# Optimization experiments

Measured on AMD Instinct MI355X. Metric: run time of the kernel, lower is better.

Reference implementation:

```python
import jax, jax.numpy as jnp
import numpy as np

B, N, M, D = 32, 500, 500, 256
SQRT_D = 16.0
LOGIT_CLIP = 10.0


def setup_inputs() -> dict:
    key = jax.random.key(0)
    ks = jax.random.split(key, 12)
    s = 1.0 / np.sqrt(D)
    return {
        "encoded_q0": jax.random.normal(ks[0], (B, N, D), jnp.float32),
        "encoded_jobs": jax.random.normal(ks[1], (B, M, D), jnp.float32),
        "encoded_q1": jax.random.normal(ks[2], (B, N, D), jnp.float32),
        "cur_cost_mat": jax.random.uniform(ks[3], (B, N, M), jnp.float32),
        "log_scale": jnp.ones((1,), jnp.float32),
        "ninf_mask": jnp.zeros((B, N, M), jnp.float32),
        "Wq0": jax.random.normal(ks[4], (D, D), jnp.float32) * s,
        "Wq1": jax.random.normal(ks[5], (D, D), jnp.float32) * s,
        "Wk": jax.random.normal(ks[6], (D, D), jnp.float32) * s,
        "Wv": jax.random.normal(ks[7], (D, D), jnp.float32) * s,
        "alpha1": jnp.ones((1,), jnp.float32),
        "alpha2": jnp.ones((1,), jnp.float32),
    }


def reference(encoded_q0, encoded_jobs, encoded_q1, cur_cost_mat, log_scale,
              ninf_mask, Wq0, Wq1, Wk, Wv, alpha1, alpha2):
    # precomputed state (set_kv / set_q1): Linear without bias -> x @ W.T
    k = jnp.einsum('bmd,ed->bme', encoded_jobs, Wk)
    v = jnp.einsum('bmd,ed->bme', encoded_jobs, Wv)
    q1 = jnp.einsum('bnd,ed->bne', encoded_q1, Wq1)
    q0 = jnp.einsum('bnd,ed->bne', encoded_q0, Wq0)
    q = q1 + q0

    # AAFM: adaptation bias = -alpha1 * log_scale * cost (+ ninf_mask)
    exp_bias = jnp.exp(-alpha1 * log_scale * cur_cost_mat + ninf_mask)  # (B,N,M)
    exp_k = jnp.exp(k)                                                   # (B,M,D)
    num = jnp.einsum('bnm,bmd->bnd', exp_bias, exp_k * v)
    den = jnp.einsum('bnm,bmd->bnd', exp_bias, exp_k)
    weighted = jnp.nan_to_num(num / den)
    aafm_out = jax.nn.sigmoid(q) * weighted                              # (B,N,D)

    # single-head scoring against raw encoded_jobs
    score = jnp.einsum('bnd,bmd->bnm', aafm_out, encoded_jobs)
    score = score / SQRT_D - alpha2 * log_scale * cur_cost_mat
    score = LOGIT_CLIP * jnp.tanh(score) + ninf_mask
    return jax.nn.softmax(score, axis=-1)
```

## Files before the change

### kernel.cpp

```cpp
#include <hip/hip_runtime.h>
#include <math.h>

using u16 = unsigned short;
typedef __attribute__((ext_vector_type(8))) short short8;
typedef __attribute__((ext_vector_type(16))) float floatx16;

constexpr int Bc = 32, Nn = 500, Mm = 500, Dd = 256;
constexpr float LOGIT_CLIP = 10.0f;
constexpr float INV_SQRT_D = 1.0f / 16.0f;

__device__ __forceinline__ floatx16 mfma32(short8 a, short8 b, floatx16 c) {
    return __builtin_amdgcn_mfma_f32_32x32x16_bf16(a, b, c, 0, 0, 0);
}

__device__ __forceinline__ floatx16 zero16() {
    floatx16 v = {0.f,0.f,0.f,0.f,0.f,0.f,0.f,0.f,0.f,0.f,0.f,0.f,0.f,0.f,0.f,0.f};
    return v;
}

__device__ __forceinline__ void gl_lds16(const u16* g, u16* l) {
    __builtin_amdgcn_global_load_lds(
        (const __attribute__((address_space(1))) unsigned int*)g,
        (__attribute__((address_space(3))) unsigned int*)l, 16, 0, 0);
}

__device__ __forceinline__ void split1(float x, u16& h, u16& l) {
    unsigned u = __float_as_uint(x);
    unsigned rh = (u + 0x7FFFu + ((u >> 16) & 1u)) & 0xFFFF0000u;
    float fh = __uint_as_float(rh);
    float fl = x - fh;
    unsigned ul = __float_as_uint(fl);
    unsigned rl = ul + 0x7FFFu + ((ul >> 16) & 1u);
    h = (u16)(rh >> 16);
    l = (u16)(rl >> 16);
}

__device__ __forceinline__ u16 bf16rtn(float x) {
    unsigned u = __float_as_uint(x);
    return (u16)((u + 0x7FFFu + ((u >> 16) & 1u)) >> 16);
}

__device__ __forceinline__ float fast_tanh(float x) {
    return 1.0f - 2.0f / (__expf(2.0f * x) + 1.0f);
}

__device__ __forceinline__ void split8(const float4& a, const float4& c,
                                       short8& hv, short8& lv) {
    u16 hh, ll;
    split1(a.x, hh, ll); hv[0] = (short)hh; lv[0] = (short)ll;
    split1(a.y, hh, ll); hv[1] = (short)hh; lv[1] = (short)ll;
    split1(a.z, hh, ll); hv[2] = (short)hh; lv[2] = (short)ll;
    split1(a.w, hh, ll); hv[3] = (short)hh; lv[3] = (short)ll;
    split1(c.x, hh, ll); hv[4] = (short)hh; lv[4] = (short)ll;
    split1(c.y, hh, ll); hv[5] = (short)hh; lv[5] = (short)ll;
    split1(c.z, hh, ll); hv[6] = (short)hh; lv[6] = (short)ll;
    split1(c.w, hh, ll); hv[7] = (short)hh; lv[7] = (short)ll;
}


__global__ __launch_bounds__(256) void k0w_pk(const float* __restrict__ s0,
                                              const float* __restrict__ s1,
                                              const float* __restrict__ s2,
                                              const float* __restrict__ s3,
                                              u16* __restrict__ pkw) {
    const float* s = blockIdx.y == 0 ? s0 : blockIdx.y == 1 ? s1 :
                     blockIdx.y == 2 ? s2 : s3;
    const int w = blockIdx.y;
    const int flat = (blockIdx.x * 256 + threadIdx.x) * 8;
    const int i = flat >> 8, j0 = flat & 255;
    float4 a = *(const float4*)&s[flat];
    float4 c = *(const float4*)&s[flat + 4];
    short8 hv, lv;
    split8(a, c, hv, lv);
    const int dt = i >> 5, i31 = i & 31, dc = j0 >> 4, hp = (j0 >> 3) & 1;
    const size_t off = (size_t)(w * 8 + dt) * 16384 + (size_t)dc * 1024
                     + (size_t)((hp << 5) | i31) * 8;
    *(short8*)&pkw[off] = hv;
    *(short8*)&pkw[off + 512] = lv;
}

__global__ __launch_bounds__(256) void k0pkj(const float* __restrict__ s,
                                             u16* __restrict__ d) {
    const int bx = blockIdx.x;
    const int b = bx >> 6;
    const int chunk = bx & 63;
    const int flat = threadIdx.x * 8;
    const int lr = flat >> 8;
    const int j0 = flat & 255;
    const int pr = chunk * 8 + lr;
    short8 hv = {0,0,0,0,0,0,0,0}, lv = {0,0,0,0,0,0,0,0};
    if (pr < Nn) {
        const size_t o = ((size_t)b * Nn + pr) * Dd + j0;
        float4 a = *(const float4*)&s[o];
        float4 c = *(const float4*)&s[o + 4];
        split8(a, c, hv, lv);
    }
    const int mt = pr >> 5, r31 = pr & 31;
    const int dc = j0 >> 4, hp = (j0 >> 3) & 1;
    const size_t off = (size_t)(b * 16 + mt) * 16384 + (size_t)dc * 1024
                     + (size_t)((hp << 5) | r31) * 8;
    *(short8*)&d[off] = hv;
    *(short8*)&d[off + 512] = lv;
}

__global__ __launch_bounds__(256) void k1_kv(const u16* __restrict__ pkj,
                                             const u16* __restrict__ pkw,
                                             u16* __restrict__ pkb) {
    const int lane = threadIdx.x & 63, wv = threadIdx.x >> 6;
    const int l31 = lane & 31, h = lane >> 5;
    const int b = blockIdx.z;
    const int dt = blockIdx.y * 4 + wv;
    const int mt = blockIdx.x;
    const int M0 = mt * 32;

    const size_t wk  = (size_t)dt * 16384 + (size_t)lane * 8;
    const size_t wvb = (size_t)(8 + dt) * 16384 + (size_t)lane * 8;
    const size_t jb  = (size_t)(b * 16 + mt) * 16384 + (size_t)lane * 8;

    floatx16 ak = zero16(), av = zero16();

    short8 buf[3][6];
#define K1L(S, DC) { \
    buf[S][0] = *(const short8*)(pkw + wk  + (size_t)(DC) * 1024); \
    buf[S][1] = *(const short8*)(pkw + wk  + (size_t)(DC) * 1024 + 512); \
    buf[S][2] = *(const short8*)(pkw + wvb + (size_t)(DC) * 1024); \
    buf[S][3] = *(const short8*)(pkw + wvb + (size_t)(DC) * 1024 + 512); \
    buf[S][4] = *(const short8*)(pkj + jb  + (size_t)(DC) * 1024); \
    buf[S][5] = *(const short8*)(pkj + jb  + (size_t)(DC) * 1024 + 512); }

    K1L(0, 0)
    K1L(1, 1)
#pragma unroll
    for (int it = 0; it < 16; ++it) {
        if (it + 2 < 16) { K1L((it + 2) % 3, it + 2) }
        const int c = it % 3;
        ak = mfma32(buf[c][0], buf[c][4], ak);
        ak = mfma32(buf[c][0], buf[c][5], ak);
        ak = mfma32(buf[c][1], buf[c][4], ak);
        av = mfma32(buf[c][2], buf[c][4], av);
        av = mfma32(buf[c][2], buf[c][5], av);
        av = mfma32(buf[c][3], buf[c][4], av);
    }
#undef K1L

    const int hp = (l31 >> 3) & 1, ee = l31 & 7, mcl = l31 >> 4;
    const size_t sb0 = ((size_t)b * 8 + dt) * 65536
                     + (size_t)(mt * 2 + mcl) * 2048 + (size_t)hp * 256 + ee;
    const bool v0 = (M0 + l31) < Mm;
#pragma unroll
    for (int r = 0; r < 16; ++r) {
        const int d31 = (r & 3) + ((r >> 2) << 3) + (h << 2);
        const size_t o = sb0 + (size_t)d31 * 8;
        u16 hh, ll;
        const float ek = v0 ? __expf(ak[r]) : 0.f;
        const float ev = v0 ? ek * av[r] : 0.f;
        split1(ek, hh, ll); pkb[o] = hh; pkb[o + 512] = ll;
        split1(ev, hh, ll); pkb[o + 1024] = hh; pkb[o + 1536] = ll;
    }
}

__global__ __launch_bounds__(256) void k2_q(const float* __restrict__ q0,
                                            const float* __restrict__ q1,
                                            const u16* __restrict__ pkw,
                                            float* __restrict__ sq) {
    __shared__ u16 tq[4][32][264];
    const int t = threadIdx.x;
    const int lane = t & 63, wv = t >> 6;
    const int l31 = lane & 31, h = lane >> 5;
    const int b = blockIdx.y;
    const int nt = blockIdx.x;

#pragma unroll
    for (int s = 0; s < 2; ++s) {
        const float* src = s ? q1 : q0;
#pragma unroll
        for (int it = 0; it < 4; ++it) {
            const int flat = (it * 256 + t) * 8;
            const int nl = flat >> 8, j0 = flat & 255;
            const int n = min(nt * 32 + nl, Nn - 1);
            const size_t o = ((size_t)b * Nn + n) * Dd + j0;
            float4 a = *(const float4*)&src[o];
            float4 c = *(const float4*)&src[o + 4];
            short8 hv, lv;
            split8(a, c, hv, lv);
            *(short8*)&tq[s * 2][nl][j0] = hv;
            *(short8*)&tq[s * 2 + 1][nl][j0] = lv;
        }
    }
    __syncthreads();

    const int dt0 = wv;
    const int dt1 = wv + 4;
    const size_t w00 = (size_t)(16 + dt0) * 16384 + (size_t)lane * 8;
    const size_t w10 = (size_t)(24 + dt0) * 16384 + (size_t)lane * 8;
    const size_t w01 = (size_t)(16 + dt1) * 16384 + (size_t)lane * 8;
    const size_t w11 = (size_t)(24 + dt1) * 16384 + (size_t)lane * 8;

    floatx16 acc0 = zero16(), acc1 = zero16();

    short8 buf[3][8];
#define K2L(S, DC) { \
    buf[S][0] = *(const short8*)(pkw + w00 + (size_t)(DC) * 1024); \
    buf[S][1] = *(const short8*)(pkw + w00 + (size_t)(DC) * 1024 + 512); \
    buf[S][2] = *(const short8*)(pkw + w10 + (size_t)(DC) * 1024); \
    buf[S][3] = *(const short8*)(pkw + w10 + (size_t)(DC) * 1024 + 512); \
    buf[S][4] = *(const short8*)(pkw + w01 + (size_t)(DC) * 1024); \
    buf[S][5] = *(const short8*)(pkw + w01 + (size_t)(DC) * 1024 + 512); \
    buf[S][6] = *(const short8*)(pkw + w11 + (size_t)(DC) * 1024); \
    buf[S][7] = *(const short8*)(pkw + w11 + (size_t)(DC) * 1024 + 512); }

    K2L(0, 0)
    K2L(1, 1)
#pragma unroll
    for (int it = 0; it < 16; ++it) {
        if (it + 2 < 16) { K2L((it + 2) % 3, it + 2) }
        const int c = it % 3;
        const int co = it * 16 + h * 8;
        short8 a0h = *(const short8*)&tq[0][l31][co];
        short8 a0l = *(const short8*)&tq[1][l31][co];
        short8 a1h = *(const short8*)&tq[2][l31][co];
        short8 a1l = *(const short8*)&tq[3][l31][co];
        acc0 = mfma32(a0h, buf[c][0], acc0);
        acc0 = mfma32(a0h, buf[c][1], acc0);
        acc0 = mfma32(a0l, buf[c][0], acc0);
        acc0 = mfma32(a1h, buf[c][2], acc0);
        acc0 = mfma32(a1h, buf[c][3], acc0);
        acc0 = mfma32(a1l, buf[c][2], acc0);
        acc1 = mfma32(a0h, buf[c][4], acc1);
        acc1 = mfma32(a0h, buf[c][5], acc1);
        acc1 = mfma32(a0l, buf[c][4], acc1);
        acc1 = mfma32(a1h, buf[c][6], acc1);
        acc1 = mfma32(a1h, buf[c][7], acc1);
        acc1 = mfma32(a1l, buf[c][6], acc1);
    }
#undef K2L

    float* sp0 = sq + ((((size_t)b * 16 + nt) * 8 + dt0) * 64 + lane) * 16;
    float* sp1 = sq + ((((size_t)b * 16 + nt) * 8 + dt1) * 64 + lane) * 16;
#pragma unroll
    for (int r = 0; r < 16; ++r) {
        sp0[r] = 1.0f / (1.0f + __expf(-acc0[r]));
        sp1[r] = 1.0f / (1.0f + __expf(-acc1[r]));
    }
}

__global__ __launch_bounds__(256) void k3_aafm(const float* __restrict__ cost,
                                               const float* __restrict__ mask,
                                               const float* __restrict__ alpha1,
                                               const float* __restrict__ lsc,
                                               const u16* __restrict__ pkb,
                                               const float* __restrict__ sq,
                                               u16* __restrict__ pkc) {
    __shared__ u16 tile[32][520];
    __shared__ u16 bbuf[2][8192];
    const int i = blockIdx.x;
    const int x = i & 7, j = i >> 3;
    const int nt = j & 15;
    const int dh = (j >> 4) & 1;
    const int b = ((j >> 5) << 3) + x;
    const int t = threadIdx.x;
    const int lane = t & 63, wv = t >> 6;
    const int l31 = lane & 31, h = lane >> 5;
    const int N0 = nt << 5;
    const int dt = dh * 4 + wv;

    const u16* pbB = pkb + ((size_t)b * 8 + dh * 4) * 65536;

#define STG3(BUF, MC) { \
    { const int f = 0 * 2048 + t * 8; \
      gl_lds16(pbB + (size_t)(f >> 11) * 65536 + (size_t)(MC) * 2048 + (f & 2047), \
               &bbuf[BUF][0 * 2048 + wv * 512]); } \
    { const int f = 1 * 2048 + t * 8; \
      gl_lds16(pbB + (size_t)(f >> 11) * 65536 + (size_t)(MC) * 2048 + (f & 2047), \
               &bbuf[BUF][1 * 2048 + wv * 512]); } \
    { const int f = 2 * 2048 + t * 8; \
      gl_lds16(pbB + (size_t)(f >> 11) * 65536 + (size_t)(MC) * 2048 + (f & 2047), \
               &bbuf[BUF][2 * 2048 + wv * 512]); } \
    { const int f = 3 * 2048 + t * 8; \
      gl_lds16(pbB + (size_t)(f >> 11) * 65536 + (size_t)(MC) * 2048 + (f & 2047), \
               &bbuf[BUF][3 * 2048 + wv * 512]); } }

    STG3(0, 0)

    const float a1ls = alpha1[0] * lsc[0];
#pragma unroll
    for (int q = 0; q < 8; ++q) {
        const int flat = (q << 11) + (t << 3);
        const int nl = flat >> 9, m = flat & 511;
        const int n = min(N0 + nl, Nn - 1);
        const size_t o = ((size_t)b * Nn + n) * Mm + m;
        ushort4 w0 = {0, 0, 0, 0}, w1 = {0, 0, 0, 0};
        if (m <= 488) {
            float4 c0 = *(const float4*)&cost[o];
            float4 c1 = *(const float4*)&cost[o + 4];
            float4 k0 = *(const float4*)&mask[o];
            float4 k1 = *(const float4*)&mask[o + 4];
            w0.x = bf16rtn(__expf(fmaf(-a1ls, c0.x, k0.x)));
            w0.y = bf16rtn(__expf(fmaf(-a1ls, c0.y, k0.y)));
            w0.z = bf16rtn(__expf(fmaf(-a1ls, c0.z, k0.z)));
            w0.w = bf16rtn(__expf(fmaf(-a1ls, c0.w, k0.w)));
            w1.x = bf16rtn(__expf(fmaf(-a1ls, c1.x, k1.x)));
            w1.y = bf16rtn(__expf(fmaf(-a1ls, c1.y, k1.y)));
            w1.z = bf16rtn(__expf(fmaf(-a1ls, c1.z, k1.z)));
            w1.w = bf16rtn(__expf(fmaf(-a1ls, c1.w, k1.w)));
        } else if (m == 496) {
            float4 c0 = *(const float4*)&cost[o];
            float4 k0 = *(const float4*)&mask[o];
            w0.x = bf16rtn(__expf(fmaf(-a1ls, c0.x, k0.x)));
            w0.y = bf16rtn(__expf(fmaf(-a1ls, c0.y, k0.y)));
            w0.z = bf16rtn(__expf(fmaf(-a1ls, c0.z, k0.z)));
            w0.w = bf16rtn(__expf(fmaf(-a1ls, c0.w, k0.w)));
        }
        *(ushort4*)&tile[nl][m] = w0;
        *(ushort4*)&tile[nl][m + 4] = w1;
    }
    __syncthreads();

    floatx16 dn = zero16(), nm = zero16();
#pragma unroll
    for (int mc = 0; mc < 32; ++mc) {
        const int cur = mc & 1, nxt = cur ^ 1;
        if (mc + 1 < 32) { STG3(nxt, mc + 1) }
        short8 aa = *(const short8*)&tile[l31][mc * 16 + h * 8];
        const u16* bp = &bbuf[cur][wv * 2048];
        short8 ekh = *(const short8*)(bp + (size_t)lane * 8);
        short8 ekl = *(const short8*)(bp + 512 + (size_t)lane * 8);
        short8 evh = *(const short8*)(bp + 1024 + (size_t)lane * 8);
        short8 evl = *(const short8*)(bp + 1536 + (size_t)lane * 8);
        dn = mfma32(aa, ekh, dn);
        dn = mfma32(aa, ekl, dn);
        nm = mfma32(aa, evh, nm);
        nm = mfma32(aa, evl, nm);
        __syncthreads();
    }
#undef STG3

    const float* sp = sq + ((((size_t)b * 16 + nt) * 8 + dt) * 64 + lane) * 16;
    const int hp = (l31 >> 3) & 1, ee = l31 & 7;
    const int dcol = dt * 32 + l31;
    const int dc0 = dcol >> 4;
    const size_t cb0 = (size_t)(b * 16 + nt) * 16384 + (size_t)dc0 * 1024
                     + (size_t)hp * 256 + ee;
#pragma unroll
    for (int r = 0; r < 16; ++r) {
        const int n31 = (r & 3) + ((r >> 2) << 3) + (h << 2);
        const int n = N0 + n31;
        if (n < Nn) {
            const size_t o = cb0 + (size_t)n31 * 8;
            u16 hh, ll;
            const float d0 = dn[r];
            const float w0 = (d0 != 0.f) ? nm[r] / d0 : 0.f;
            split1(sp[r] * w0, hh, ll);
            pkc[o] = hh; pkc[o + 512] = ll;
        }
    }
}

__global__ __launch_bounds__(512) void k4_score(const u16* __restrict__ pkc,
                                                const u16* __restrict__ pkj,
                                                const float* __restrict__ cost,
                                                const float* __restrict__ mask,
                                                const float* __restrict__ alpha2,
                                                const float* __restrict__ lsc,
                                                float* __restrict__ out) {
    __shared__ u16 bb[2][16384];
    float (*pred)[8] = (float(*)[8])bb;
    const int i = blockIdx.x;
    const int x = i & 7, j = i >> 3;
    const int nt = j & 15;
    const int b = ((j >> 4) << 3) + x;
    const int t = threadIdx.x;
    const int lane = t & 63, wv = t >> 6;
    const int l31 = lane & 31, h = lane >> 5;
    const int N0 = nt << 5;
    const float a2ls = alpha2[0] * lsc[0];

    const u16* jbB = pkj + (size_t)b * 16 * 16384;
    const size_t ab = (size_t)(b * 16 + nt) * 16384 + (size_t)lane * 8;
    const int m0g = wv * 64 + l31;
    const int m1g = m0g + 32;

    floatx16 acc0 = zero16(), acc1 = zero16();

#define STG4(BUF, DC) { \
    { const int f = 0 * 4096 + t * 8; \
      gl_lds16(jbB + (size_t)(f >> 10) * 16384 + (size_t)(DC) * 1024 + (f & 1023), \
               &bb[BUF][0 * 4096 + wv * 512]); } \
    { const int f = 1 * 4096 + t * 8; \
      gl_lds16(jbB + (size_t)(f >> 10) * 16384 + (size_t)(DC) * 1024 + (f & 1023), \
               &bb[BUF][1 * 4096 + wv * 512]); } \
    { const int f = 2 * 4096 + t * 8; \
      gl_lds16(jbB + (size_t)(f >> 10) * 16384 + (size_t)(DC) * 1024 + (f & 1023), \
               &bb[BUF][2 * 4096 + wv * 512]); } \
    { const int f = 3 * 4096 + t * 8; \
      gl_lds16(jbB + (size_t)(f >> 10) * 16384 + (size_t)(DC) * 1024 + (f & 1023), \
               &bb[BUF][3 * 4096 + wv * 512]); } }

    STG4(0, 0)
    short8 aH[2], aL[2];
    aH[0] = *(const short8*)(pkc + ab);
    aL[0] = *(const short8*)(pkc + ab + 512);
    __syncthreads();
#pragma unroll
    for (int dc = 0; dc < 16; ++dc) {
        const int cur = dc & 1, nxt = cur ^ 1;
        if (dc + 1 < 16) {
            STG4(nxt, dc + 1)
            aH[nxt] = *(const short8*)(pkc + ab + (size_t)(dc + 1) * 1024);
            aL[nxt] = *(const short8*)(pkc + ab + (size_t)(dc + 1) * 1024 + 512);
        }
        const u16* bp = &bb[cur][wv * 2048];
        short8 b0h = *(const short8*)(bp + (size_t)lane * 8);
        short8 b0l = *(const short8*)(bp + 512 + (size_t)lane * 8);
        short8 b1h = *(const short8*)(bp + 1024 + (size_t)lane * 8);
        short8 b1l = *(const short8*)(bp + 1536 + (size_t)lane * 8);
        acc0 = mfma32(aH[cur], b0h, acc0);
        acc0 = mfma32(aH[cur], b0l, acc0);
        acc0 = mfma32(aL[cur], b0h, acc0);
        acc1 = mfma32(aH[cur], b1h, acc1);
        acc1 = mfma32(aH[cur], b1l, acc1);
        acc1 = mfma32(aL[cur], b1h, acc1);
        __syncthreads();
    }
#undef STG4

    float lg0[16], lg1[16];
    const size_t cb = (size_t)b * Nn * Mm;
#pragma unroll
    for (int r = 0; r < 16; ++r) {
        const int row = (r & 3) + ((r >> 2) << 3) + (h << 2);
        const int n = N0 + row;
        if (n < Nn) {
            const size_t o = cb + (size_t)n * Mm + m0g;
            lg0[r] = LOGIT_CLIP * fast_tanh(fmaf(-a2ls, cost[o], acc0[r] * INV_SQRT_D)) + mask[o];
            if (m1g < Mm) {
                const size_t o1 = o + 32;
                lg1[r] = LOGIT_CLIP * fast_tanh(fmaf(-a2ls, cost[o1], acc1[r] * INV_SQRT_D)) + mask[o1];
            } else lg1[r] = -1e30f;
        } else { lg0[r] = -1e30f; lg1[r] = -1e30f; }
    }

    float rm[16];
#pragma unroll
    for (int r = 0; r < 16; ++r) rm[r] = fmaxf(lg0[r], lg1[r]);
#pragma unroll
    for (int d = 1; d < 32; d <<= 1)
#pragma unroll
        for (int r = 0; r < 16; ++r) rm[r] = fmaxf(rm[r], __shfl_xor(rm[r], d));
    if (l31 == 0) {
#pragma unroll
        for (int r = 0; r < 16; ++r)
            pred[(r & 3) + ((r >> 2) << 3) + (h << 2)][wv] = rm[r];
    }
    __syncthreads();
    float fm[16];
#pragma unroll
    for (int r = 0; r < 16; ++r) {
        const int row = (r & 3) + ((r >> 2) << 3) + (h << 2);
        float v = pred[row][0];
#pragma unroll
        for (int w = 1; w < 8; ++w) v = fmaxf(v, pred[row][w]);
        fm[r] = v;
    }
    __syncthreads();

    float sm[16];
#pragma unroll
    for (int r = 0; r < 16; ++r) {
        lg0[r] = __expf(lg0[r] - fm[r]);
        lg1[r] = __expf(lg1[r] - fm[r]);
        sm[r] = lg0[r] + lg1[r];
    }
#pragma unroll
    for (int d = 1; d < 32; d <<= 1)
#pragma unroll
        for (int r = 0; r < 16; ++r) sm[r] += __shfl_xor(sm[r], d);
    if (l31 == 0) {
#pragma unroll
        for (int r = 0; r < 16; ++r)
            pred[(r & 3) + ((r >> 2) << 3) + (h << 2)][wv] = sm[r];
    }
    __syncthreads();

#pragma unroll
    for (int r = 0; r < 16; ++r) {
        const int row = (r & 3) + ((r >> 2) << 3) + (h << 2);
        const int n = N0 + row;
        if (n < Nn) {
            float s = pred[row][0];
#pragma unroll
            for (int w = 1; w < 8; ++w) s += pred[row][w];
            const float inv = 1.0f / s;
            const size_t o = cb + (size_t)n * Mm + m0g;
            out[o] = lg0[r] * inv;
            if (m1g < Mm) out[o + 32] = lg1[r] * inv;
        }
    }
}

extern "C" void kernel_launch(void* const* d_in, const int* in_sizes, int n_in,
                              void* d_out, int out_size, void* d_ws, size_t ws_size,
                              hipStream_t stream) {
    const float* q0        = (const float*)d_in[0];
    const float* jobs      = (const float*)d_in[1];
    const float* q1        = (const float*)d_in[2];
    const float* cost      = (const float*)d_in[3];
    const float* log_scale = (const float*)d_in[4];
    const float* mask      = (const float*)d_in[5];
    const float* Wq0       = (const float*)d_in[6];
    const float* Wq1       = (const float*)d_in[7];
    const float* Wk        = (const float*)d_in[8];
    const float* Wv        = (const float*)d_in[9];
    const float* alpha1    = (const float*)d_in[10];
    const float* alpha2    = (const float*)d_in[11];
    float* out = (float*)d_out;

    const size_t PK_SZ  = (size_t)Bc * 16 * 16384;
    const size_t PKW_SZ = (size_t)4 * 8 * 16384;
    const size_t PKB_SZ = (size_t)Bc * 8 * 65536;
    const size_t SQ_SZ  = (size_t)Bc * 16 * 8 * 64 * 16;

    u16* ws   = (u16*)d_ws;
    u16* pkj  = ws;
    u16* pkw  = ws + PK_SZ;
    u16* pkb  = pkw + PKW_SZ;
    float* sq = (float*)(pkb + PKB_SZ);
    u16* pkc  = (u16*)(sq + SQ_SZ);
    (void)ws_size;

    dim3 blk(256);
    k0w_pk<<<dim3(32, 4), blk, 0, stream>>>(Wk, Wv, Wq0, Wq1, pkw);
    k0pkj<<<2048, blk, 0, stream>>>(jobs, pkj);
    k1_kv<<<dim3(16, 2, 32), blk, 0, stream>>>(pkj, pkw, pkb);
    k2_q<<<dim3(16, 32), blk, 0, stream>>>(q0, q1, pkw, sq);
    k3_aafm<<<1024, blk, 0, stream>>>(cost, mask, alpha1, log_scale, pkb, sq, pkc);
    k4_score<<<512, dim3(512), 0, stream>>>(pkc, pkj, cost, mask,
                                            alpha2, log_scale, out);
}
```

Baseline: 299.2 us.

## Fuse AAFM and scoring kernels, keep aafm_out in LDS, load B operands directly

Merges the AAFM kernel and the score/softmax kernel into one 512-thread kernel per (batch, 32-row tile). The sigmoid-gated weighted result stays in shared memory instead of round-tripping through the global pkc buffer, which removes one launch and the associated global writes and reads. B-operand staging through global_load_lds double buffers is replaced by direct per-lane register loads with a three-deep prefetch ring, which also drops the per-iteration barriers. The risks are lower occupancy from the larger blocks and register ring, and half as many blocks for the AAFM stage.

```diff
diff --git a/kernel.cpp b/kernel.cpp
--- a/kernel.cpp
+++ b/kernel.cpp
@@ -16,12 +16,6 @@
 __device__ __forceinline__ floatx16 zero16() {
     floatx16 v = {0.f,0.f,0.f,0.f,0.f,0.f,0.f,0.f,0.f,0.f,0.f,0.f,0.f,0.f,0.f,0.f};
     return v;
-}
-
-__device__ __forceinline__ void gl_lds16(const u16* g, u16* l) {
-    __builtin_amdgcn_global_load_lds(
-        (const __attribute__((address_space(1))) unsigned int*)g,
-        (__attribute__((address_space(3))) unsigned int*)l, 16, 0, 0);
 }
 
 __device__ __forceinline__ void split1(float x, u16& h, u16& l) {
@@ -244,48 +238,30 @@
     }
 }
 
-__global__ __launch_bounds__(256) void k3_aafm(const float* __restrict__ cost,
-                                               const float* __restrict__ mask,
-                                               const float* __restrict__ alpha1,
-                                               const float* __restrict__ lsc,
-                                               const u16* __restrict__ pkb,
-                                               const float* __restrict__ sq,
-                                               u16* __restrict__ pkc) {
-    __shared__ u16 tile[32][520];
-    __shared__ u16 bbuf[2][8192];
+__global__ __launch_bounds__(512) void k34(const float* __restrict__ cost,
+                                           const float* __restrict__ mask,
+                                           const float* __restrict__ alpha1,
+                                           const float* __restrict__ alpha2,
+                                           const float* __restrict__ lsc,
+                                           const u16* __restrict__ pkb,
+                                           const u16* __restrict__ pkj,
+                                           const float* __restrict__ sq,
+                                           float* __restrict__ out) {
+    __shared__ u16 sh[16640];
+    __shared__ float pred[32][8];
     const int i = blockIdx.x;
     const int x = i & 7, j = i >> 3;
     const int nt = j & 15;
-    const int dh = (j >> 4) & 1;
-    const int b = ((j >> 5) << 3) + x;
+    const int b = ((j >> 4) << 3) + x;
     const int t = threadIdx.x;
     const int lane = t & 63, wv = t >> 6;
     const int l31 = lane & 31, h = lane >> 5;
     const int N0 = nt << 5;
-    const int dt = dh * 4 + wv;
-
-    const u16* pbB = pkb + ((size_t)b * 8 + dh * 4) * 65536;
-
-#define STG3(BUF, MC) { \
-    { const int f = 0 * 2048 + t * 8; \
-      gl_lds16(pbB + (size_t)(f >> 11) * 65536 + (size_t)(MC) * 2048 + (f & 2047), \
-               &bbuf[BUF][0 * 2048 + wv * 512]); } \
-    { const int f = 1 * 2048 + t * 8; \
-      gl_lds16(pbB + (size_t)(f >> 11) * 65536 + (size_t)(MC) * 2048 + (f & 2047), \
-               &bbuf[BUF][1 * 2048 + wv * 512]); } \
-    { const int f = 2 * 2048 + t * 8; \
-      gl_lds16(pbB + (size_t)(f >> 11) * 65536 + (size_t)(MC) * 2048 + (f & 2047), \
-               &bbuf[BUF][2 * 2048 + wv * 512]); } \
-    { const int f = 3 * 2048 + t * 8; \
-      gl_lds16(pbB + (size_t)(f >> 11) * 65536 + (size_t)(MC) * 2048 + (f & 2047), \
-               &bbuf[BUF][3 * 2048 + wv * 512]); } }
-
-    STG3(0, 0)
 
     const float a1ls = alpha1[0] * lsc[0];
 #pragma unroll
-    for (int q = 0; q < 8; ++q) {
-        const int flat = (q << 11) + (t << 3);
+    for (int q = 0; q < 4; ++q) {
+        const int flat = (q << 12) + (t << 3);
         const int nl = flat >> 9, m = flat & 511;
         const int n = min(N0 + nl, Nn - 1);
         const size_t o = ((size_t)b * Nn + n) * Mm + m;
@@ -311,120 +287,84 @@
             w0.z = bf16rtn(__expf(fmaf(-a1ls, c0.z, k0.z)));
             w0.w = bf16rtn(__expf(fmaf(-a1ls, c0.w, k0.w)));
         }
-        *(ushort4*)&tile[nl][m] = w0;
-        *(ushort4*)&tile[nl][m + 4] = w1;
-    }
-    __syncthreads();
-
+        *(ushort4*)&sh[nl * 520 + m] = w0;
+        *(ushort4*)&sh[nl * 520 + m + 4] = w1;
+    }
+    __syncthreads();
+
+    const size_t bbase = ((size_t)b * 8 + wv) * 65536 + (size_t)lane * 8;
     floatx16 dn = zero16(), nm = zero16();
+    short8 buf[3][4];
+#define K3L(S, MC) { \
+    buf[S][0] = *(const short8*)(pkb + bbase + (size_t)(MC) * 2048); \
+    buf[S][1] = *(const short8*)(pkb + bbase + (size_t)(MC) * 2048 + 512); \
+    buf[S][2] = *(const short8*)(pkb + bbase + (size_t)(MC) * 2048 + 1024); \
+    buf[S][3] = *(const short8*)(pkb + bbase + (size_t)(MC) * 2048 + 1536); }
+
+    K3L(0, 0)
+    K3L(1, 1)
 #pragma unroll
     for (int mc = 0; mc < 32; ++mc) {
-        const int cur = mc & 1, nxt = cur ^ 1;
-        if (mc + 1 < 32) { STG3(nxt, mc + 1) }
-        short8 aa = *(const short8*)&tile[l31][mc * 16 + h * 8];
-        const u16* bp = &bbuf[cur][wv * 2048];
-        short8 ekh = *(const short8*)(bp + (size_t)lane * 8);
-        short8 ekl = *(const short8*)(bp + 512 + (size_t)lane * 8);
-        short8 evh = *(const short8*)(bp + 1024 + (size_t)lane * 8);
-        short8 evl = *(const short8*)(bp + 1536 + (size_t)lane * 8);
-        dn = mfma32(aa, ekh, dn);
-        dn = mfma32(aa, ekl, dn);
-        nm = mfma32(aa, evh, nm);
-        nm = mfma32(aa, evl, nm);
-        __syncthreads();
-    }
-#undef STG3
-
-    const float* sp = sq + ((((size_t)b * 16 + nt) * 8 + dt) * 64 + lane) * 16;
-    const int hp = (l31 >> 3) & 1, ee = l31 & 7;
-    const int dcol = dt * 32 + l31;
-    const int dc0 = dcol >> 4;
-    const size_t cb0 = (size_t)(b * 16 + nt) * 16384 + (size_t)dc0 * 1024
-                     + (size_t)hp * 256 + ee;
-#pragma unroll
-    for (int r = 0; r < 16; ++r) {
-        const int n31 = (r & 3) + ((r >> 2) << 3) + (h << 2);
-        const int n = N0 + n31;
-        if (n < Nn) {
-            const size_t o = cb0 + (size_t)n31 * 8;
-            u16 hh, ll;
+        if (mc + 2 < 32) { K3L((mc + 2) % 3, mc + 2) }
+        const int c = mc % 3;
+        short8 aa = *(const short8*)&sh[l31 * 520 + mc * 16 + h * 8];
+        dn = mfma32(aa, buf[c][0], dn);
+        dn = mfma32(aa, buf[c][1], dn);
+        nm = mfma32(aa, buf[c][2], nm);
+        nm = mfma32(aa, buf[c][3], nm);
+    }
+#undef K3L
+    __syncthreads();
+
+    {
+        const float* sp = sq + ((((size_t)b * 16 + nt) * 8 + wv) * 64 + lane) * 16;
+        const int hp = (l31 >> 3) & 1, ee = l31 & 7;
+        const int fo = (wv * 2 + (l31 >> 4)) * 1024 + hp * 256 + ee;
+#pragma unroll
+        for (int r = 0; r < 16; ++r) {
+            const int n31 = (r & 3) + ((r >> 2) << 3) + (h << 2);
             const float d0 = dn[r];
             const float w0 = (d0 != 0.f) ? nm[r] / d0 : 0.f;
+            u16 hh, ll;
             split1(sp[r] * w0, hh, ll);
-            pkc[o] = hh; pkc[o + 512] = ll;
+            sh[fo + n31 * 8] = hh;
+            sh[fo + 512 + n31 * 8] = ll;
         }
     }
-}
-
-__global__ __launch_bounds__(512) void k4_score(const u16* __restrict__ pkc,
-                                                const u16* __restrict__ pkj,
-                                                const float* __restrict__ cost,
-                                                const float* __restrict__ mask,
-                                                const float* __restrict__ alpha2,
-                                                const float* __restrict__ lsc,
-                                                float* __restrict__ out) {
-    __shared__ u16 bb[2][16384];
-    float (*pred)[8] = (float(*)[8])bb;
-    const int i = blockIdx.x;
-    const int x = i & 7, j = i >> 3;
-    const int nt = j & 15;
-    const int b = ((j >> 4) << 3) + x;
-    const int t = threadIdx.x;
-    const int lane = t & 63, wv = t >> 6;
-    const int l31 = lane & 31, h = lane >> 5;
-    const int N0 = nt << 5;
-    const float a2ls = alpha2[0] * lsc[0];
-
-    const u16* jbB = pkj + (size_t)b * 16 * 16384;
-    const size_t ab = (size_t)(b * 16 + nt) * 16384 + (size_t)lane * 8;
+    __syncthreads();
+
+    const u16* jb0p = pkj + ((size_t)b * 16 + wv * 2) * 16384 + (size_t)lane * 8;
+    const u16* jb1p = jb0p + 16384;
     const int m0g = wv * 64 + l31;
     const int m1g = m0g + 32;
 
     floatx16 acc0 = zero16(), acc1 = zero16();
-
-#define STG4(BUF, DC) { \
-    { const int f = 0 * 4096 + t * 8; \
-      gl_lds16(jbB + (size_t)(f >> 10) * 16384 + (size_t)(DC) * 1024 + (f & 1023), \
-               &bb[BUF][0 * 4096 + wv * 512]); } \
-    { const int f = 1 * 4096 + t * 8; \
-      gl_lds16(jbB + (size_t)(f >> 10) * 16384 + (size_t)(DC) * 1024 + (f & 1023), \
-               &bb[BUF][1 * 4096 + wv * 512]); } \
-    { const int f = 2 * 4096 + t * 8; \
-      gl_lds16(jbB + (size_t)(f >> 10) * 16384 + (size_t)(DC) * 1024 + (f & 1023), \
-               &bb[BUF][2 * 4096 + wv * 512]); } \
-    { const int f = 3 * 4096 + t * 8; \
-      gl_lds16(jbB + (size_t)(f >> 10) * 16384 + (size_t)(DC) * 1024 + (f & 1023), \
-               &bb[BUF][3 * 4096 + wv * 512]); } }
-
-    STG4(0, 0)
-    short8 aH[2], aL[2];
-    aH[0] = *(const short8*)(pkc + ab);
-    aL[0] = *(const short8*)(pkc + ab + 512);
-    __syncthreads();
+    short8 jbuf[3][4];
+#define K4L(S, DC) { \
+    jbuf[S][0] = *(const short8*)(jb0p + (size_t)(DC) * 1024); \
+    jbuf[S][1] = *(const short8*)(jb0p + (size_t)(DC) * 1024 + 512); \
+    jbuf[S][2] = *(const short8*)(jb1p + (size_t)(DC) * 1024); \
+    jbuf[S][3] = *(const short8*)(jb1p + (size_t)(DC) * 1024 + 512); }
+
+    K4L(0, 0)
+    K4L(1, 1)
 #pragma unroll
     for (int dc = 0; dc < 16; ++dc) {
-        const int cur = dc & 1, nxt = cur ^ 1;
-        if (dc + 1 < 16) {
-            STG4(nxt, dc + 1)
-            aH[nxt] = *(const short8*)(pkc + ab + (size_t)(dc + 1) * 1024);
-            aL[nxt] = *(const short8*)(pkc + ab + (size_t)(dc + 1) * 1024 + 512);
-        }
-        const u16* bp = &bb[cur][wv * 2048];
-        short8 b0h = *(const short8*)(bp + (size_t)lane * 8);
-        short8 b0l = *(const short8*)(bp + 512 + (size_t)lane * 8);
-        short8 b1h = *(const short8*)(bp + 1024 + (size_t)lane * 8);
-        short8 b1l = *(const short8*)(bp + 1536 + (size_t)lane * 8);
-        acc0 = mfma32(aH[cur], b0h, acc0);
-        acc0 = mfma32(aH[cur], b0l, acc0);
-        acc0 = mfma32(aL[cur], b0h, acc0);
-        acc1 = mfma32(aH[cur], b1h, acc1);
-        acc1 = mfma32(aH[cur], b1l, acc1);
-        acc1 = mfma32(aL[cur], b1h, acc1);
-        __syncthreads();
-    }
-#undef STG4
+        if (dc + 2 < 16) { K4L((dc + 2) % 3, dc + 2) }
+        const int c = dc % 3;
+        short8 aH = *(const short8*)&sh[dc * 1024 + lane * 8];
+        short8 aL = *(const short8*)&sh[dc * 1024 + 512 + lane * 8];
+        acc0 = mfma32(aH, jbuf[c][0], acc0);
+        acc0 = mfma32(aH, jbuf[c][1], acc0);
+        acc0 = mfma32(aL, jbuf[c][0], acc0);
+        acc1 = mfma32(aH, jbuf[c][2], acc1);
+        acc1 = mfma32(aH, jbuf[c][3], acc1);
+        acc1 = mfma32(aL, jbuf[c][2], acc1);
+    }
+#undef K4L
 
     float lg0[16], lg1[16];
+    const float a2ls = alpha2[0] * lsc[0];
     const size_t cb = (size_t)b * Nn * Mm;
 #pragma unroll
     for (int r = 0; r < 16; ++r) {
@@ -518,14 +458,12 @@
     const size_t PK_SZ  = (size_t)Bc * 16 * 16384;
     const size_t PKW_SZ = (size_t)4 * 8 * 16384;
     const size_t PKB_SZ = (size_t)Bc * 8 * 65536;
-    const size_t SQ_SZ  = (size_t)Bc * 16 * 8 * 64 * 16;
 
     u16* ws   = (u16*)d_ws;
     u16* pkj  = ws;
     u16* pkw  = ws + PK_SZ;
     u16* pkb  = pkw + PKW_SZ;
     float* sq = (float*)(pkb + PKB_SZ);
-    u16* pkc  = (u16*)(sq + SQ_SZ);
     (void)ws_size;
 
     dim3 blk(256);
@@ -533,7 +471,6 @@
     k0pkj<<<2048, blk, 0, stream>>>(jobs, pkj);
     k1_kv<<<dim3(16, 2, 32), blk, 0, stream>>>(pkj, pkw, pkb);
     k2_q<<<dim3(16, 32), blk, 0, stream>>>(q0, q1, pkw, sq);
-    k3_aafm<<<1024, blk, 0, stream>>>(cost, mask, alpha1, log_scale, pkb, sq, pkc);
-    k4_score<<<512, dim3(512), 0, stream>>>(pkc, pkj, cost, mask,
-                                            alpha2, log_scale, out);
-}
+    k34<<<512, dim3(512), 0, stream>>>(cost, mask, alpha1, alpha2, log_scale,
+                                       pkb, pkj, sq, out);
+}
```

Result: faster. 273.4 us (-8.6%).
